# Performance work log

Hardware: AMD Instinct MI355X
Metric: run time of the kernel (lower is better)

## Reference

```python
import jax, jax.numpy as jnp
import numpy as np

EMB = 128
SQRT_EMB = 128 ** 0.5
LOGIT_CLIP = 10.0


def setup_inputs() -> dict:
    key = jax.random.key(0)
    ks = jax.random.split(key, 10)
    B, N, M, D = 128, 512, 512, EMB
    s = 1.0 / np.sqrt(D)
    return {
        "encoded_last_node": jax.random.normal(ks[0], (B, N, D), jnp.float32),
        "load": jax.random.uniform(ks[1], (B, N), jnp.float32),
        "cur_dist": jax.random.uniform(ks[2], (B, N, M), jnp.float32),
        "log_scale": jnp.ones((), jnp.float32),
        "ninf_mask": jnp.zeros((B, N, M), jnp.float32),
        "encoded_nodes": jax.random.normal(ks[3], (B, M, D), jnp.float32),
        "Wq_last": jax.random.normal(ks[4], (D, D + 1), jnp.float32) * s,
        "Wk": jax.random.normal(ks[5], (D, D), jnp.float32) * s,
        "Wv": jax.random.normal(ks[6], (D, D), jnp.float32) * s,
        "alpha1": jnp.ones((1,), jnp.float32),
        "alpha2": jnp.ones((1,), jnp.float32),
    }


def reference(encoded_last_node, load, cur_dist, log_scale, ninf_mask,
              encoded_nodes, Wq_last, Wk, Wv, alpha1, alpha2):
    # set_kv
    k = jnp.einsum('bmd,ed->bme', encoded_nodes, Wk)   # (B,M,D)
    v = jnp.einsum('bmd,ed->bme', encoded_nodes, Wv)   # (B,M,D)
    # query from last node + load
    input_cat = jnp.concatenate([encoded_last_node, load[:, :, None]], axis=2)  # (B,N,D+1)
    q = jnp.einsum('bnc,ec->bne', input_cat, Wq_last)  # (B,N,D)
    # AAFM: exp-bias linear attention with sigmoid gate
    adaptation_bias = -alpha1[0] * log_scale * cur_dist + ninf_mask  # (B,N,M)
    eb = jnp.exp(adaptation_bias)
    ek = jnp.exp(k)
    num = jnp.einsum('bnm,bmd->bnd', eb, ek * v)
    den = jnp.einsum('bnm,bmd->bnd', eb, ek)
    weighted = jnp.nan_to_num(num / den)  # mirrors torch nan_to_num correction
    aafm_out = jax.nn.sigmoid(q) * weighted  # (B,N,D)
    # single-head decode score against encoder embeddings
    score = jnp.einsum('bnd,bmd->bnm', aafm_out, encoded_nodes)
    score_scaled = score / SQRT_EMB - alpha2[0] * log_scale * cur_dist
    score_masked = LOGIT_CLIP * jnp.tanh(score_scaled) + ninf_mask
    probs = jax.nn.softmax(score_masked, axis=-1)
    return probs
```

## Files before the change

kernel.cpp:

```cpp
#include <hip/hip_runtime.h>
#include <math.h>

#define B 128
#define N 512
#define M 512
#define D 128

typedef __attribute__((ext_vector_type(8))) short s16x8;
typedef __attribute__((ext_vector_type(4))) short s16x4;
typedef __attribute__((ext_vector_type(4))) float f32x4;

#define MFMA16(a, b, c) __builtin_amdgcn_mfma_f32_16x16x32_bf16(a, b, c, 0, 0, 0)

__device__ __forceinline__ void gload16(const void* g, void* l) {
    __builtin_amdgcn_global_load_lds(
        (const __attribute__((address_space(1))) unsigned int*)g,
        (__attribute__((address_space(3))) unsigned int*)l, 16, 0, 0);
}

__device__ __forceinline__ float fast_tanh(float x) {
    x = fminf(fmaxf(x, -15.f), 15.f);
    float E = __expf(2.f * x);
    return 1.f - 2.f / (E + 1.f);
}

__device__ __forceinline__ unsigned short bf16rne(float x) {
    unsigned u = __float_as_uint(x);
    return (unsigned short)((u + 0x7FFF + ((u >> 16) & 1)) >> 16);
}

__device__ __forceinline__ void fsplit(float x, short& h, short& l) {
    unsigned u = __float_as_uint(x);
    h = (short)(u >> 16);
    float fh = __uint_as_float(u & 0xffff0000u);
    l = (short)(__float_as_uint(x - fh) >> 16);
}

__device__ __forceinline__ void fsplit8(float4 x0, float4 x1, s16x8& h, s16x8& l) {
    short a, b;
    fsplit(x0.x, a, b); h[0] = a; l[0] = b;
    fsplit(x0.y, a, b); h[1] = a; l[1] = b;
    fsplit(x0.z, a, b); h[2] = a; l[2] = b;
    fsplit(x0.w, a, b); h[3] = a; l[3] = b;
    fsplit(x1.x, a, b); h[4] = a; l[4] = b;
    fsplit(x1.y, a, b); h[5] = a; l[5] = b;
    fsplit(x1.z, a, b); h[6] = a; l[6] = b;
    fsplit(x1.w, a, b); h[7] = a; l[7] = b;
}

__device__ __forceinline__ void ebpack(float4 c0, float4 c1, float4 f0, float4 f1,
                                       float a1ls, s16x8& a) {
    a[0] = (short)bf16rne(__expf(fmaf(-a1ls, c0.x, f0.x)));
    a[1] = (short)bf16rne(__expf(fmaf(-a1ls, c0.y, f0.y)));
    a[2] = (short)bf16rne(__expf(fmaf(-a1ls, c0.z, f0.z)));
    a[3] = (short)bf16rne(__expf(fmaf(-a1ls, c0.w, f0.w)));
    a[4] = (short)bf16rne(__expf(fmaf(-a1ls, c1.x, f1.x)));
    a[5] = (short)bf16rne(__expf(fmaf(-a1ls, c1.y, f1.y)));
    a[6] = (short)bf16rne(__expf(fmaf(-a1ls, c1.z, f1.z)));
    a[7] = (short)bf16rne(__expf(fmaf(-a1ls, c1.w, f1.w)));
}

__global__ void k_prep_w(const float* __restrict__ Wk, const float* __restrict__ Wv,
                         const float* __restrict__ Wq,
                         unsigned short* __restrict__ Wk_hi, unsigned short* __restrict__ Wk_lo,
                         unsigned short* __restrict__ Wv_hi, unsigned short* __restrict__ Wv_lo,
                         unsigned short* __restrict__ Wq_hi, unsigned short* __restrict__ Wq_lo) {
    int i = blockIdx.x * 256 + threadIdx.x;
    short h, l;
    if (i < 16384) {
        fsplit(Wk[i], h, l); Wk_hi[i] = (unsigned short)h; Wk_lo[i] = (unsigned short)l;
    } else if (i < 32768) {
        int j = i - 16384;
        fsplit(Wv[j], h, l); Wv_hi[j] = (unsigned short)h; Wv_lo[j] = (unsigned short)l;
    } else {
        int j = i - 32768; int e = j >> 7, d = j & 127;
        fsplit(Wq[e * 129 + d], h, l); Wq_hi[j] = (unsigned short)h; Wq_lo[j] = (unsigned short)l;
    }
}

__global__ __launch_bounds__(256) void k_kv(const float* __restrict__ enc,
        const unsigned short* __restrict__ Wk_hi, const unsigned short* __restrict__ Wk_lo,
        const unsigned short* __restrict__ Wv_hi, const unsigned short* __restrict__ Wv_lo,
        unsigned short* __restrict__ EKb, unsigned short* __restrict__ EKVb) {
    int b = blockIdx.y;
    int wave = threadIdx.x >> 6, lane = threadIdx.x & 63;
    int row = lane & 15, kg = lane >> 4;
    int m0 = blockIdx.x * 64 + wave * 16;
    f32x4 acc[16];
#pragma unroll
    for (int i = 0; i < 16; i++) acc[i] = (f32x4)0.f;
    const float* ap = enc + ((size_t)b * M + m0 + row) * D + kg * 8;
#pragma unroll
    for (int ks = 0; ks < 4; ks++) {
        float4 x0 = *(const float4*)(ap + ks * 32);
        float4 x1 = *(const float4*)(ap + ks * 32 + 4);
        s16x8 ah, al;
        fsplit8(x0, x1, ah, al);
        int wb = ks * 32 + kg * 8;
#pragma unroll
        for (int ct = 0; ct < 8; ct++) {
            int e = ct * 16 + row;
            s16x8 bh = *(const s16x8*)(Wk_hi + e * D + wb);
            s16x8 bl = *(const s16x8*)(Wk_lo + e * D + wb);
            acc[ct] = MFMA16(ah, bh, acc[ct]);
            acc[ct] = MFMA16(al, bh, acc[ct]);
            acc[ct] = MFMA16(ah, bl, acc[ct]);
            bh = *(const s16x8*)(Wv_hi + e * D + wb);
            bl = *(const s16x8*)(Wv_lo + e * D + wb);
            acc[8 + ct] = MFMA16(ah, bh, acc[8 + ct]);
            acc[8 + ct] = MFMA16(al, bh, acc[8 + ct]);
            acc[8 + ct] = MFMA16(ah, bl, acc[8 + ct]);
        }
    }
#pragma unroll
    for (int ct = 0; ct < 8; ct++) {
        int e = ct * 16 + row;
        s16x4 kb, vb;
#pragma unroll
        for (int r = 0; r < 4; r++) {
            float ek = __expf(acc[ct][r]);
            float ev = ek * acc[8 + ct][r];
            kb[r] = (short)bf16rne(ek);
            vb[r] = (short)bf16rne(ev);
        }
        int m = m0 + kg * 4;
        int chunk = (m & 31) >> 3;
        int p = chunk ^ (e & 3);
        size_t o = ((size_t)b * D + e) * M + (size_t)(m & ~31) + p * 8 + (m & 7);
        *(s16x4*)(EKb + o) = kb;
        *(s16x4*)(EKVb + o) = vb;
    }
}

__global__ void k_encsplit(const float* __restrict__ enc,
                           unsigned short* __restrict__ Eh, unsigned short* __restrict__ El) {
    size_t i = (size_t)blockIdx.x * 256 + threadIdx.x;
    size_t bm = i >> 4;
    int c = (int)(i & 15);
    int m = (int)(bm & 511);
    int p = c ^ (m & 7);
    const float* src = enc + bm * 128 + c * 8;
    float4 x0 = *(const float4*)(src);
    float4 x1 = *(const float4*)(src + 4);
    s16x8 h, l;
    fsplit8(x0, x1, h, l);
    *(s16x8*)(Eh + bm * 128 + p * 8) = h;
    *(s16x8*)(El + bm * 128 + p * 8) = l;
}

__global__ __launch_bounds__(256, 3) void k_fused(
        const float* __restrict__ encl, const float* __restrict__ loadv,
        const float* __restrict__ Wq,
        const unsigned short* __restrict__ Wq_hi, const unsigned short* __restrict__ Wq_lo,
        const float* __restrict__ cd, const float* __restrict__ ninf,
        const unsigned short* __restrict__ EKVb, const unsigned short* __restrict__ EKb,
        const unsigned short* __restrict__ Eh, const unsigned short* __restrict__ El,
        const float* __restrict__ a1p, const float* __restrict__ a2p,
        const float* __restrict__ lsp, float* __restrict__ out) {
    int o = blockIdx.x;
    int xcd = o & 7, j = o >> 3;
    int b = ((j >> 4) << 3) + xcd;
    int nb = j & 15;
    int n0 = nb * 32;
    int w = threadIdx.x >> 6, lane = threadIdx.x & 63;
    int row = lane & 15, kg = lane >> 4;
    int ng = w >> 1, mh = w & 1;
    __shared__ __align__(16) char lds[2][16384];
    __shared__ float redm[32][2], reds[32][2];
    float a1ls = a1p[0] * lsp[0];
    float a2ls = a2p[0] * lsp[0];
    const float invs = 0.08838834764831845f;

    f32x4 sqa[2][2];
#pragma unroll
    for (int s = 0; s < 2; s++)
#pragma unroll
        for (int ct = 0; ct < 2; ct++) sqa[s][ct] = (f32x4)0.f;
#pragma unroll
    for (int s = 0; s < 2; s++) {
        const float* ap = encl + ((size_t)b * N + n0 + s * 16 + row) * D + kg * 8;
#pragma unroll
        for (int ks = 0; ks < 4; ks++) {
            float4 x0 = *(const float4*)(ap + ks * 32);
            float4 x1 = *(const float4*)(ap + ks * 32 + 4);
            s16x8 ah, al;
            fsplit8(x0, x1, ah, al);
            int wb = ks * 32 + kg * 8;
#pragma unroll
            for (int ct = 0; ct < 2; ct++) {
                int e = w * 32 + ct * 16 + row;
                s16x8 bh = *(const s16x8*)(Wq_hi + e * D + wb);
                s16x8 bl = *(const s16x8*)(Wq_lo + e * D + wb);
                sqa[s][ct] = MFMA16(ah, bh, sqa[s][ct]);
                sqa[s][ct] = MFMA16(al, bh, sqa[s][ct]);
                sqa[s][ct] = MFMA16(ah, bl, sqa[s][ct]);
            }
        }
    }
    float sqv[2][2][4];
#pragma unroll
    for (int s = 0; s < 2; s++)
#pragma unroll
        for (int ct = 0; ct < 2; ct++) {
            int e = w * 32 + ct * 16 + row;
            float wcol = Wq[e * 129 + 128];
#pragma unroll
            for (int r = 0; r < 4; r++) {
                int n = n0 + s * 16 + kg * 4 + r;
                float q = sqa[s][ct][r] + loadv[(size_t)b * N + n] * wcol;
                sqv[s][ct][r] = 1.f / (1.f + __expf(-q));
            }
        }

    f32x4 accN[2][2], accD[2][2];
#pragma unroll
    for (int s = 0; s < 2; s++)
#pragma unroll
        for (int i = 0; i < 2; i++) { accN[s][i] = (f32x4)0.f; accD[s][i] = (f32x4)0.f; }
    const char* gEKV = (const char*)EKVb + (size_t)b * D * M * 2;
    const char* gEK  = (const char*)EKb  + (size_t)b * D * M * 2;
    const float* cdp0 = cd + ((size_t)b * N + n0 + row) * M + kg * 8;
    const float* nfp0 = ninf + ((size_t)b * N + n0 + row) * M + kg * 8;
    const float* cdp1 = cdp0 + (size_t)16 * M;
    const float* nfp1 = nfp0 + (size_t)16 * M;
    int rbase = w * 2048 + row * 64 + ((kg ^ (row & 3)) << 4);

#define STAGE_ND(ldsbase, mt)                                                    \
    _Pragma("unroll")                                                            \
    for (int jv = 0; jv < 4; jv++) {                                             \
        int idx = jv * 256 + threadIdx.x;                                        \
        const char* gb = (idx >> 9) ? gEK : gEKV;                                \
        int rem = idx & 511;                                                     \
        gload16(gb + (size_t)(rem >> 2) * 1024 + (size_t)(mt) * 64 + (rem & 3) * 16, \
                (char*)(ldsbase) + idx * 16);                                    \
    }

    float4 c00 = *(const float4*)(cdp0), c01 = *(const float4*)(cdp0 + 4);
    float4 f00 = *(const float4*)(nfp0), f01 = *(const float4*)(nfp0 + 4);
    float4 c10 = *(const float4*)(cdp1), c11 = *(const float4*)(cdp1 + 4);
    float4 f10 = *(const float4*)(nfp1), f11 = *(const float4*)(nfp1 + 4);
    STAGE_ND((char*)lds, 0)

#pragma unroll 2
    for (int mt = 0; mt < 16; mt++) {
        int cur = mt & 1;
        __syncthreads();
        s16x8 a0, a1;
        ebpack(c00, c01, f00, f01, a1ls, a0);
        ebpack(c10, c11, f10, f11, a1ls, a1);
        if (mt < 15) {
            int m = (mt + 1) * 32;
            c00 = *(const float4*)(cdp0 + m); c01 = *(const float4*)(cdp0 + m + 4);
            f00 = *(const float4*)(nfp0 + m); f01 = *(const float4*)(nfp0 + m + 4);
            c10 = *(const float4*)(cdp1 + m); c11 = *(const float4*)(cdp1 + m + 4);
            f10 = *(const float4*)(nfp1 + m); f11 = *(const float4*)(nfp1 + m + 4);
            STAGE_ND((char*)lds + (cur ^ 1) * 16384, mt + 1)
        }
        const char* L = (const char*)lds + cur * 16384;
#pragma unroll
        for (int ct = 0; ct < 2; ct++) {
            int ro = ct * 1024 + rbase;
            s16x8 bv = *(const s16x8*)(L + ro);
            s16x8 bk = *(const s16x8*)(L + 8192 + ro);
            accN[0][ct] = MFMA16(a0, bv, accN[0][ct]);
            accN[1][ct] = MFMA16(a1, bv, accN[1][ct]);
            accD[0][ct] = MFMA16(a0, bk, accD[0][ct]);
            accD[1][ct] = MFMA16(a1, bk, accD[1][ct]);
        }
    }

    float* af = (float*)lds;
#pragma unroll
    for (int s = 0; s < 2; s++)
#pragma unroll
        for (int ct = 0; ct < 2; ct++) {
            int e = w * 32 + ct * 16 + row;
#pragma unroll
            for (int r = 0; r < 4; r++) {
                int nl = s * 16 + kg * 4 + r;
                float num = accN[s][ct][r], den = accD[s][ct][r];
                float ww = (den != 0.f) ? num / den : 0.f;
                float aafm = sqv[s][ct][r] * ww;
                unsigned u = __float_as_uint(aafm);
                unsigned hi = u >> 16;
                float fh = __uint_as_float(u & 0xffff0000u);
                unsigned lo = __float_as_uint(aafm - fh) >> 16;
                af[nl * 128 + e] = __uint_as_float(hi | (lo << 16));
            }
        }
    __syncthreads();
    s16x8 ah[4], al[4];
#pragma unroll
    for (int es = 0; es < 4; es++) {
        const float* src = af + (ng * 16 + row) * 128 + es * 32 + kg * 8;
        float4 w0 = *(const float4*)(src);
        float4 w1 = *(const float4*)(src + 4);
        unsigned u;
        u = __float_as_uint(w0.x); ah[es][0] = (short)(u & 0xffff); al[es][0] = (short)(u >> 16);
        u = __float_as_uint(w0.y); ah[es][1] = (short)(u & 0xffff); al[es][1] = (short)(u >> 16);
        u = __float_as_uint(w0.z); ah[es][2] = (short)(u & 0xffff); al[es][2] = (short)(u >> 16);
        u = __float_as_uint(w0.w); ah[es][3] = (short)(u & 0xffff); al[es][3] = (short)(u >> 16);
        u = __float_as_uint(w1.x); ah[es][4] = (short)(u & 0xffff); al[es][4] = (short)(u >> 16);
        u = __float_as_uint(w1.y); ah[es][5] = (short)(u & 0xffff); al[es][5] = (short)(u >> 16);
        u = __float_as_uint(w1.z); ah[es][6] = (short)(u & 0xffff); al[es][6] = (short)(u >> 16);
        u = __float_as_uint(w1.w); ah[es][7] = (short)(u & 0xffff); al[es][7] = (short)(u >> 16);
    }
    __syncthreads();

    f32x4 acc[16];
#pragma unroll
    for (int i = 0; i < 16; i++) acc[i] = (f32x4)0.f;
    int mloc = mh * 16 + row;
    int rb2 = mloc * 256;
    int sw = mloc & 7;
    size_t rowidx[4];
#pragma unroll
    for (int r = 0; r < 4; r++)
        rowidx[r] = ((size_t)b * N + n0 + ng * 16 + kg * 4 + r) * M;

#define STAGE_SC(ldsbase, mc)                                                      \
    _Pragma("unroll")                                                              \
    for (int jv = 0; jv < 4; jv++) {                                               \
        int id = (w * 4 + jv) * 64 + lane;                                         \
        int arr = id >> 9, rem = id & 511;                                         \
        const unsigned short* gb = arr ? El : Eh;                                  \
        gload16((const char*)gb + ((size_t)b * M + (size_t)(mc) * 32) * 256 + rem * 16, \
                (char*)(ldsbase) + arr * 8192 + rem * 16);                         \
    }

    STAGE_SC((char*)lds, 0)
#pragma unroll
    for (int mc = 0; mc < 16; mc++) {
        int cur = mc & 1;
        __syncthreads();
        const char* L = (const char*)lds + cur * 16384;
#pragma unroll
        for (int es = 0; es < 4; es++) {
            int ph = (4 * es + kg) ^ sw;
            s16x8 bh = *(const s16x8*)(L + rb2 + ph * 16);
            s16x8 bl = *(const s16x8*)(L + 8192 + rb2 + ph * 16);
            acc[mc] = MFMA16(ah[es], bh, acc[mc]);
            acc[mc] = MFMA16(al[es], bh, acc[mc]);
            acc[mc] = MFMA16(ah[es], bl, acc[mc]);
        }
        float cdv[4], nfv[4];
#pragma unroll
        for (int r = 0; r < 4; r++) {
            size_t idx = rowidx[r] + (size_t)mc * 32 + mloc;
            cdv[r] = cd[idx];
            nfv[r] = ninf[idx];
        }
        if (mc < 15) STAGE_SC((char*)lds + (cur ^ 1) * 16384, mc + 1)
#pragma unroll
        for (int r = 0; r < 4; r++) {
            acc[mc][r] = 10.f * fast_tanh(fmaf(acc[mc][r], invs, -a2ls * cdv[r]))
                       + nfv[r];
        }
    }
    float mx[4], sm[4];
#pragma unroll
    for (int r = 0; r < 4; r++) {
        float m = acc[0][r];
#pragma unroll
        for (int a = 1; a < 16; a++) m = fmaxf(m, acc[a][r]);
#pragma unroll
        for (int s = 1; s < 16; s <<= 1) m = fmaxf(m, __shfl_xor(m, s, 64));
        mx[r] = m;
    }
    int rl = ng * 16 + kg * 4;
    if (row == 0) {
#pragma unroll
        for (int r = 0; r < 4; r++) redm[rl + r][mh] = mx[r];
    }
    __syncthreads();
#pragma unroll
    for (int r = 0; r < 4; r++) {
        float m = fmaxf(redm[rl + r][0], redm[rl + r][1]);
        float s = 0.f;
#pragma unroll
        for (int a = 0; a < 16; a++) {
            float e = __expf(acc[a][r] - m);
            acc[a][r] = e;
            s += e;
        }
#pragma unroll
        for (int sh = 1; sh < 16; sh <<= 1) s += __shfl_xor(s, sh, 64);
        sm[r] = s;
    }
    if (row == 0) {
#pragma unroll
        for (int r = 0; r < 4; r++) reds[rl + r][mh] = sm[r];
    }
    __syncthreads();
#pragma unroll
    for (int r = 0; r < 4; r++) {
        float inv = 1.f / (reds[rl + r][0] + reds[rl + r][1]);
        size_t ro = ((size_t)b * N + n0 + rl + r) * M;
#pragma unroll
        for (int a = 0; a < 16; a++) {
            out[ro + a * 32 + mh * 16 + row] = acc[a][r] * inv;
        }
    }
}

extern "C" void kernel_launch(void* const* d_in, const int* in_sizes, int n_in,
                              void* d_out, int out_size, void* d_ws, size_t ws_size,
                              hipStream_t stream) {
    const float* encl  = (const float*)d_in[0];
    const float* loadv = (const float*)d_in[1];
    const float* cdist = (const float*)d_in[2];
    const float* ls    = (const float*)d_in[3];
    const float* ninf  = (const float*)d_in[4];
    const float* enc   = (const float*)d_in[5];
    const float* Wq    = (const float*)d_in[6];
    const float* Wk    = (const float*)d_in[7];
    const float* Wv    = (const float*)d_in[8];
    const float* a1    = (const float*)d_in[9];
    const float* a2    = (const float*)d_in[10];
    char* ws = (char*)d_ws;
    unsigned short* EKb     = (unsigned short*)(ws);
    unsigned short* EKVb    = (unsigned short*)(ws + 16777216);
    unsigned short* ENC_hi  = (unsigned short*)(ws + 33554432);
    unsigned short* ENC_lo  = (unsigned short*)(ws + 50331648);
    unsigned short* Wk_hi   = (unsigned short*)(ws + 67108864);
    unsigned short* Wk_lo   = (unsigned short*)(ws + 67108864 + 32768);
    unsigned short* Wv_hi   = (unsigned short*)(ws + 67108864 + 65536);
    unsigned short* Wv_lo   = (unsigned short*)(ws + 67108864 + 98304);
    unsigned short* Wq_hi   = (unsigned short*)(ws + 67108864 + 131072);
    unsigned short* Wq_lo   = (unsigned short*)(ws + 67108864 + 163840);
    float* out = (float*)d_out;

    k_prep_w<<<192, 256, 0, stream>>>(Wk, Wv, Wq, Wk_hi, Wk_lo, Wv_hi, Wv_lo, Wq_hi, Wq_lo);
    k_kv<<<dim3(8, 128), 256, 0, stream>>>(enc, Wk_hi, Wk_lo, Wv_hi, Wv_lo, EKb, EKVb);
    k_encsplit<<<4096, 256, 0, stream>>>(enc, ENC_hi, ENC_lo);
    k_fused<<<2048, 256, 0, stream>>>(encl, loadv, Wq, Wq_hi, Wq_lo,
                                      cdist, ninf, EKVb, EKb, ENC_hi, ENC_lo,
                                      a1, a2, ls, out);
}
```

Before: 363.1 us.

## Use per-wave LDS staging with manual vmcnt pipelining and single-bf16 encoder operand

Each wave now owns a private LDS slice and stages its own tiles with a two-deep prefetch, synchronised by explicit s_waitcnt vmcnt/lgkmcnt counts instead of block-wide __syncthreads in both the attention and score loops. The score phase is repartitioned so each wave handles all 32 rows over its own 128-column slice. The encoder embedding is packed to a single bf16 copy rather than a hi/lo split, which drops one MFMA per step and halves the staged bytes. This lowers the precision of the score matmul, and the hand-counted waitcnt values are fragile if the compiler reorders memory operations.

```diff
diff --git a/kernel.cpp b/kernel.cpp
--- a/kernel.cpp
+++ b/kernel.cpp
@@ -11,6 +11,14 @@
 typedef __attribute__((ext_vector_type(4))) float f32x4;
 
 #define MFMA16(a, b, c) __builtin_amdgcn_mfma_f32_16x16x32_bf16(a, b, c, 0, 0, 0)
+
+#define FENCE()   asm volatile("" ::: "memory")
+#define VMCNT4()  asm volatile("s_waitcnt vmcnt(4)" ::: "memory")
+#define VMCNT8()  asm volatile("s_waitcnt vmcnt(8)" ::: "memory")
+#define VMCNT12() asm volatile("s_waitcnt vmcnt(12)" ::: "memory")
+#define VMCNT20() asm volatile("s_waitcnt vmcnt(20)" ::: "memory")
+#define LGKMCNT0() asm volatile("s_waitcnt lgkmcnt(0)" ::: "memory")
+#define SCHEDBAR() __builtin_amdgcn_sched_barrier(0)
 
 __device__ __forceinline__ void gload16(const void* g, void* l) {
     __builtin_amdgcn_global_load_lds(
@@ -132,8 +140,7 @@
     }
 }
 
-__global__ void k_encsplit(const float* __restrict__ enc,
-                           unsigned short* __restrict__ Eh, unsigned short* __restrict__ El) {
+__global__ void k_encpack(const float* __restrict__ enc, unsigned short* __restrict__ Eb) {
     size_t i = (size_t)blockIdx.x * 256 + threadIdx.x;
     size_t bm = i >> 4;
     int c = (int)(i & 15);
@@ -142,10 +149,12 @@
     const float* src = enc + bm * 128 + c * 8;
     float4 x0 = *(const float4*)(src);
     float4 x1 = *(const float4*)(src + 4);
-    s16x8 h, l;
-    fsplit8(x0, x1, h, l);
-    *(s16x8*)(Eh + bm * 128 + p * 8) = h;
-    *(s16x8*)(El + bm * 128 + p * 8) = l;
+    s16x8 v;
+    v[0] = (short)bf16rne(x0.x); v[1] = (short)bf16rne(x0.y);
+    v[2] = (short)bf16rne(x0.z); v[3] = (short)bf16rne(x0.w);
+    v[4] = (short)bf16rne(x1.x); v[5] = (short)bf16rne(x1.y);
+    v[6] = (short)bf16rne(x1.z); v[7] = (short)bf16rne(x1.w);
+    *(s16x8*)(Eb + bm * 128 + p * 8) = v;
 }
 
 __global__ __launch_bounds__(256, 3) void k_fused(
@@ -154,7 +163,7 @@
         const unsigned short* __restrict__ Wq_hi, const unsigned short* __restrict__ Wq_lo,
         const float* __restrict__ cd, const float* __restrict__ ninf,
         const unsigned short* __restrict__ EKVb, const unsigned short* __restrict__ EKb,
-        const unsigned short* __restrict__ Eh, const unsigned short* __restrict__ El,
+        const unsigned short* __restrict__ Eb,
         const float* __restrict__ a1p, const float* __restrict__ a2p,
         const float* __restrict__ lsp, float* __restrict__ out) {
     int o = blockIdx.x;
@@ -164,12 +173,12 @@
     int n0 = nb * 32;
     int w = threadIdx.x >> 6, lane = threadIdx.x & 63;
     int row = lane & 15, kg = lane >> 4;
-    int ng = w >> 1, mh = w & 1;
-    __shared__ __align__(16) char lds[2][16384];
-    __shared__ float redm[32][2], reds[32][2];
+    __shared__ __align__(16) char lds[32768];
+    __shared__ float redm[32][4], reds[32][4];
     float a1ls = a1p[0] * lsp[0];
     float a2ls = a2p[0] * lsp[0];
     const float invs = 0.08838834764831845f;
+    char* wb = lds + w * 8192;
 
     f32x4 sqa[2][2];
 #pragma unroll
@@ -185,12 +194,12 @@
             float4 x1 = *(const float4*)(ap + ks * 32 + 4);
             s16x8 ah, al;
             fsplit8(x0, x1, ah, al);
-            int wb = ks * 32 + kg * 8;
+            int wqo = ks * 32 + kg * 8;
 #pragma unroll
             for (int ct = 0; ct < 2; ct++) {
                 int e = w * 32 + ct * 16 + row;
-                s16x8 bh = *(const s16x8*)(Wq_hi + e * D + wb);
-                s16x8 bl = *(const s16x8*)(Wq_lo + e * D + wb);
+                s16x8 bh = *(const s16x8*)(Wq_hi + e * D + wqo);
+                s16x8 bl = *(const s16x8*)(Wq_lo + e * D + wqo);
                 sqa[s][ct] = MFMA16(ah, bh, sqa[s][ct]);
                 sqa[s][ct] = MFMA16(al, bh, sqa[s][ct]);
                 sqa[s][ct] = MFMA16(ah, bl, sqa[s][ct]);
@@ -211,6 +220,7 @@
                 sqv[s][ct][r] = 1.f / (1.f + __expf(-q));
             }
         }
+    FENCE();
 
     f32x4 accN[2][2], accD[2][2];
 #pragma unroll
@@ -223,52 +233,63 @@
     const float* nfp0 = ninf + ((size_t)b * N + n0 + row) * M + kg * 8;
     const float* cdp1 = cdp0 + (size_t)16 * M;
     const float* nfp1 = nfp0 + (size_t)16 * M;
-    int rbase = w * 2048 + row * 64 + ((kg ^ (row & 3)) << 4);
-
-#define STAGE_ND(ldsbase, mt)                                                    \
+
+#define STAGE_B(bufptr, mt)                                                      \
     _Pragma("unroll")                                                            \
     for (int jv = 0; jv < 4; jv++) {                                             \
-        int idx = jv * 256 + threadIdx.x;                                        \
-        const char* gb = (idx >> 9) ? gEK : gEKV;                                \
-        int rem = idx & 511;                                                     \
-        gload16(gb + (size_t)(rem >> 2) * 1024 + (size_t)(mt) * 64 + (rem & 3) * 16, \
-                (char*)(ldsbase) + idx * 16);                                    \
-    }
-
-    float4 c00 = *(const float4*)(cdp0), c01 = *(const float4*)(cdp0 + 4);
-    float4 f00 = *(const float4*)(nfp0), f01 = *(const float4*)(nfp0 + 4);
-    float4 c10 = *(const float4*)(cdp1), c11 = *(const float4*)(cdp1 + 4);
-    float4 f10 = *(const float4*)(nfp1), f11 = *(const float4*)(nfp1 + 4);
-    STAGE_ND((char*)lds, 0)
-
-#pragma unroll 2
+        int arr = jv >> 1;                                                       \
+        int rem = (jv & 1) * 64 + lane;                                          \
+        const char* gb = arr ? gEK : gEKV;                                       \
+        gload16(gb + (size_t)(w * 32 + (rem >> 2)) * 1024 + (size_t)(mt) * 64 +  \
+                    (rem & 3) * 16,                                              \
+                (char*)(bufptr) + arr * 2048 + rem * 16);                        \
+    }
+
+    float4 Ac[2][2][2], Af[2][2][2];
+#define LOAD_A(p, mt)                                                            \
+    Ac[p][0][0] = *(const float4*)(cdp0 + (mt) * 32);                            \
+    Ac[p][0][1] = *(const float4*)(cdp0 + (mt) * 32 + 4);                        \
+    Af[p][0][0] = *(const float4*)(nfp0 + (mt) * 32);                            \
+    Af[p][0][1] = *(const float4*)(nfp0 + (mt) * 32 + 4);                        \
+    Ac[p][1][0] = *(const float4*)(cdp1 + (mt) * 32);                            \
+    Ac[p][1][1] = *(const float4*)(cdp1 + (mt) * 32 + 4);                        \
+    Af[p][1][0] = *(const float4*)(nfp1 + (mt) * 32);                            \
+    Af[p][1][1] = *(const float4*)(nfp1 + (mt) * 32 + 4);
+
+    LOAD_A(0, 0) FENCE();
+    STAGE_B(wb, 0) FENCE();
+    LOAD_A(1, 1) FENCE();
+    STAGE_B(wb + 4096, 1) FENCE();
+
+    int rbB = row * 64 + ((kg ^ (row & 3)) << 4);
+#pragma unroll
     for (int mt = 0; mt < 16; mt++) {
-        int cur = mt & 1;
-        __syncthreads();
+        if (mt < 2) { VMCNT12(); } else if (mt < 15) { VMCNT20(); } else { VMCNT8(); }
+        SCHEDBAR();
+        int p = mt & 1;
         s16x8 a0, a1;
-        ebpack(c00, c01, f00, f01, a1ls, a0);
-        ebpack(c10, c11, f10, f11, a1ls, a1);
-        if (mt < 15) {
-            int m = (mt + 1) * 32;
-            c00 = *(const float4*)(cdp0 + m); c01 = *(const float4*)(cdp0 + m + 4);
-            f00 = *(const float4*)(nfp0 + m); f01 = *(const float4*)(nfp0 + m + 4);
-            c10 = *(const float4*)(cdp1 + m); c11 = *(const float4*)(cdp1 + m + 4);
-            f10 = *(const float4*)(nfp1 + m); f11 = *(const float4*)(nfp1 + m + 4);
-            STAGE_ND((char*)lds + (cur ^ 1) * 16384, mt + 1)
-        }
-        const char* L = (const char*)lds + cur * 16384;
+        ebpack(Ac[p][0][0], Ac[p][0][1], Af[p][0][0], Af[p][0][1], a1ls, a0);
+        ebpack(Ac[p][1][0], Ac[p][1][1], Af[p][1][0], Af[p][1][1], a1ls, a1);
+        const char* L = wb + p * 4096;
 #pragma unroll
         for (int ct = 0; ct < 2; ct++) {
-            int ro = ct * 1024 + rbase;
+            int ro = ct * 1024 + rbB;
             s16x8 bv = *(const s16x8*)(L + ro);
-            s16x8 bk = *(const s16x8*)(L + 8192 + ro);
+            s16x8 bk = *(const s16x8*)(L + 2048 + ro);
             accN[0][ct] = MFMA16(a0, bv, accN[0][ct]);
             accN[1][ct] = MFMA16(a1, bv, accN[1][ct]);
             accD[0][ct] = MFMA16(a0, bk, accD[0][ct]);
             accD[1][ct] = MFMA16(a1, bk, accD[1][ct]);
         }
-    }
-
+        if (mt <= 13) {
+            LGKMCNT0();
+            SCHEDBAR();
+            STAGE_B(wb + p * 4096, mt + 2) FENCE();
+            LOAD_A(p, mt + 2) FENCE();
+        }
+    }
+
+    __syncthreads();
     float* af = (float*)lds;
 #pragma unroll
     for (int s = 0; s < 2; s++)
@@ -289,118 +310,141 @@
             }
         }
     __syncthreads();
-    s16x8 ah[4], al[4];
-#pragma unroll
-    for (int es = 0; es < 4; es++) {
-        const float* src = af + (ng * 16 + row) * 128 + es * 32 + kg * 8;
-        float4 w0 = *(const float4*)(src);
-        float4 w1 = *(const float4*)(src + 4);
-        unsigned u;
-        u = __float_as_uint(w0.x); ah[es][0] = (short)(u & 0xffff); al[es][0] = (short)(u >> 16);
-        u = __float_as_uint(w0.y); ah[es][1] = (short)(u & 0xffff); al[es][1] = (short)(u >> 16);
-        u = __float_as_uint(w0.z); ah[es][2] = (short)(u & 0xffff); al[es][2] = (short)(u >> 16);
-        u = __float_as_uint(w0.w); ah[es][3] = (short)(u & 0xffff); al[es][3] = (short)(u >> 16);
-        u = __float_as_uint(w1.x); ah[es][4] = (short)(u & 0xffff); al[es][4] = (short)(u >> 16);
-        u = __float_as_uint(w1.y); ah[es][5] = (short)(u & 0xffff); al[es][5] = (short)(u >> 16);
-        u = __float_as_uint(w1.z); ah[es][6] = (short)(u & 0xffff); al[es][6] = (short)(u >> 16);
-        u = __float_as_uint(w1.w); ah[es][7] = (short)(u & 0xffff); al[es][7] = (short)(u >> 16);
-    }
+    s16x8 ah[2][4], al[2][4];
+#pragma unroll
+    for (int s = 0; s < 2; s++)
+#pragma unroll
+        for (int es = 0; es < 4; es++) {
+            const float* src = af + (s * 16 + row) * 128 + es * 32 + kg * 8;
+            float4 w0 = *(const float4*)(src);
+            float4 w1 = *(const float4*)(src + 4);
+            unsigned u;
+            u = __float_as_uint(w0.x); ah[s][es][0] = (short)(u & 0xffff); al[s][es][0] = (short)(u >> 16);
+            u = __float_as_uint(w0.y); ah[s][es][1] = (short)(u & 0xffff); al[s][es][1] = (short)(u >> 16);
+            u = __float_as_uint(w0.z); ah[s][es][2] = (short)(u & 0xffff); al[s][es][2] = (short)(u >> 16);
+            u = __float_as_uint(w0.w); ah[s][es][3] = (short)(u & 0xffff); al[s][es][3] = (short)(u >> 16);
+            u = __float_as_uint(w1.x); ah[s][es][4] = (short)(u & 0xffff); al[s][es][4] = (short)(u >> 16);
+            u = __float_as_uint(w1.y); ah[s][es][5] = (short)(u & 0xffff); al[s][es][5] = (short)(u >> 16);
+            u = __float_as_uint(w1.z); ah[s][es][6] = (short)(u & 0xffff); al[s][es][6] = (short)(u >> 16);
+            u = __float_as_uint(w1.w); ah[s][es][7] = (short)(u & 0xffff); al[s][es][7] = (short)(u >> 16);
+        }
     __syncthreads();
-
-    f32x4 acc[16];
-#pragma unroll
-    for (int i = 0; i < 16; i++) acc[i] = (f32x4)0.f;
-    int mloc = mh * 16 + row;
-    int rb2 = mloc * 256;
-    int sw = mloc & 7;
-    size_t rowidx[4];
-#pragma unroll
-    for (int r = 0; r < 4; r++)
-        rowidx[r] = ((size_t)b * N + n0 + ng * 16 + kg * 4 + r) * M;
-
-#define STAGE_SC(ldsbase, mc)                                                      \
-    _Pragma("unroll")                                                              \
-    for (int jv = 0; jv < 4; jv++) {                                               \
-        int id = (w * 4 + jv) * 64 + lane;                                         \
-        int arr = id >> 9, rem = id & 511;                                         \
-        const unsigned short* gb = arr ? El : Eh;                                  \
-        gload16((const char*)gb + ((size_t)b * M + (size_t)(mc) * 32) * 256 + rem * 16, \
-                (char*)(ldsbase) + arr * 8192 + rem * 16);                         \
-    }
-
-    STAGE_SC((char*)lds, 0)
-#pragma unroll
-    for (int mc = 0; mc < 16; mc++) {
-        int cur = mc & 1;
-        __syncthreads();
-        const char* L = (const char*)lds + cur * 16384;
+    FENCE();
+
+    f32x4 acc[2][8];
+#pragma unroll
+    for (int s = 0; s < 2; s++)
+#pragma unroll
+        for (int p = 0; p < 8; p++) acc[s][p] = (f32x4)0.f;
+    const char* gEb = (const char*)Eb + (size_t)b * M * 256;
+
+#define STAGE_D(bufptr, p)                                                       \
+    _Pragma("unroll")                                                            \
+    for (int jv = 0; jv < 4; jv++) {                                             \
+        int id = jv * 64 + lane;                                                 \
+        gload16(gEb + (size_t)(w * 128 + (p) * 16 + (id >> 4)) * 256 + (id & 15) * 16, \
+                (char*)(bufptr) + id * 16);                                      \
+    }
+
+    STAGE_D(wb, 0) FENCE();
+    STAGE_D(wb + 4096, 1) FENCE();
+
+#pragma unroll
+    for (int p = 0; p < 8; p++) {
+        if (p == 0) { VMCNT4(); } else if (p < 7) { VMCNT12(); } else { VMCNT8(); }
+        SCHEDBAR();
+        float cdv[2][4], nfv[2][4];
+#pragma unroll
+        for (int s = 0; s < 2; s++)
+#pragma unroll
+            for (int r = 0; r < 4; r++) {
+                size_t idx = ((size_t)b * N + n0 + s * 16 + kg * 4 + r) * M
+                           + (size_t)w * 128 + (size_t)p * 16 + row;
+                cdv[s][r] = cd[idx];
+                nfv[s][r] = ninf[idx];
+            }
+        FENCE();
+        const char* L = wb + (p & 1) * 4096;
+        int sw = row & 7;
 #pragma unroll
         for (int es = 0; es < 4; es++) {
             int ph = (4 * es + kg) ^ sw;
-            s16x8 bh = *(const s16x8*)(L + rb2 + ph * 16);
-            s16x8 bl = *(const s16x8*)(L + 8192 + rb2 + ph * 16);
-            acc[mc] = MFMA16(ah[es], bh, acc[mc]);
-            acc[mc] = MFMA16(al[es], bh, acc[mc]);
-            acc[mc] = MFMA16(ah[es], bl, acc[mc]);
-        }
-        float cdv[4], nfv[4];
+            s16x8 bb = *(const s16x8*)(L + row * 256 + ph * 16);
+            acc[0][p] = MFMA16(ah[0][es], bb, acc[0][p]);
+            acc[0][p] = MFMA16(al[0][es], bb, acc[0][p]);
+            acc[1][p] = MFMA16(ah[1][es], bb, acc[1][p]);
+            acc[1][p] = MFMA16(al[1][es], bb, acc[1][p]);
+        }
+        if (p <= 5) {
+            LGKMCNT0();
+            SCHEDBAR();
+            STAGE_D(wb + (p & 1) * 4096, p + 2) FENCE();
+        }
+#pragma unroll
+        for (int s = 0; s < 2; s++)
+#pragma unroll
+            for (int r = 0; r < 4; r++) {
+                acc[s][p][r] = 10.f * fast_tanh(fmaf(acc[s][p][r], invs, -a2ls * cdv[s][r]))
+                             + nfv[s][r];
+            }
+    }
+
+    float mx[2][4], sm[2][4];
+#pragma unroll
+    for (int s = 0; s < 2; s++)
 #pragma unroll
         for (int r = 0; r < 4; r++) {
-            size_t idx = rowidx[r] + (size_t)mc * 32 + mloc;
-            cdv[r] = cd[idx];
-            nfv[r] = ninf[idx];
-        }
-        if (mc < 15) STAGE_SC((char*)lds + (cur ^ 1) * 16384, mc + 1)
+            float m = acc[s][0][r];
+#pragma unroll
+            for (int p = 1; p < 8; p++) m = fmaxf(m, acc[s][p][r]);
+#pragma unroll
+            for (int sh = 1; sh < 16; sh <<= 1) m = fmaxf(m, __shfl_xor(m, sh, 64));
+            mx[s][r] = m;
+        }
+    if (row == 0) {
+#pragma unroll
+        for (int s = 0; s < 2; s++)
+#pragma unroll
+            for (int r = 0; r < 4; r++) redm[s * 16 + kg * 4 + r][w] = mx[s][r];
+    }
+    __syncthreads();
+#pragma unroll
+    for (int s = 0; s < 2; s++)
 #pragma unroll
         for (int r = 0; r < 4; r++) {
-            acc[mc][r] = 10.f * fast_tanh(fmaf(acc[mc][r], invs, -a2ls * cdv[r]))
-                       + nfv[r];
-        }
-    }
-    float mx[4], sm[4];
-#pragma unroll
-    for (int r = 0; r < 4; r++) {
-        float m = acc[0][r];
-#pragma unroll
-        for (int a = 1; a < 16; a++) m = fmaxf(m, acc[a][r]);
-#pragma unroll
-        for (int s = 1; s < 16; s <<= 1) m = fmaxf(m, __shfl_xor(m, s, 64));
-        mx[r] = m;
-    }
-    int rl = ng * 16 + kg * 4;
+            int nl = s * 16 + kg * 4 + r;
+            float m = fmaxf(fmaxf(redm[nl][0], redm[nl][1]),
+                            fmaxf(redm[nl][2], redm[nl][3]));
+            float sum = 0.f;
+#pragma unroll
+            for (int p = 0; p < 8; p++) {
+                float e = __expf(acc[s][p][r] - m);
+                acc[s][p][r] = e;
+                sum += e;
+            }
+#pragma unroll
+            for (int sh = 1; sh < 16; sh <<= 1) sum += __shfl_xor(sum, sh, 64);
+            sm[s][r] = sum;
+        }
     if (row == 0) {
 #pragma unroll
-        for (int r = 0; r < 4; r++) redm[rl + r][mh] = mx[r];
+        for (int s = 0; s < 2; s++)
+#pragma unroll
+            for (int r = 0; r < 4; r++) reds[s * 16 + kg * 4 + r][w] = sm[s][r];
     }
     __syncthreads();
 #pragma unroll
-    for (int r = 0; r < 4; r++) {
-        float m = fmaxf(redm[rl + r][0], redm[rl + r][1]);
-        float s = 0.f;
-#pragma unroll
-        for (int a = 0; a < 16; a++) {
-            float e = __expf(acc[a][r] - m);
-            acc[a][r] = e;
-            s += e;
-        }
-#pragma unroll
-        for (int sh = 1; sh < 16; sh <<= 1) s += __shfl_xor(s, sh, 64);
-        sm[r] = s;
-    }
-    if (row == 0) {
-#pragma unroll
-        for (int r = 0; r < 4; r++) reds[rl + r][mh] = sm[r];
-    }
-    __syncthreads();
-#pragma unroll
-    for (int r = 0; r < 4; r++) {
-        float inv = 1.f / (reds[rl + r][0] + reds[rl + r][1]);
-        size_t ro = ((size_t)b * N + n0 + rl + r) * M;
-#pragma unroll
-        for (int a = 0; a < 16; a++) {
-            out[ro + a * 32 + mh * 16 + row] = acc[a][r] * inv;
-        }
-    }
+    for (int s = 0; s < 2; s++)
+#pragma unroll
+        for (int r = 0; r < 4; r++) {
+            int nl = s * 16 + kg * 4 + r;
+            float inv = 1.f / (reds[nl][0] + reds[nl][1] + reds[nl][2] + reds[nl][3]);
+            size_t ro = ((size_t)b * N + n0 + nl) * M + (size_t)w * 128 + row;
+#pragma unroll
+            for (int p = 0; p < 8; p++) {
+                out[ro + p * 16] = acc[s][p][r] * inv;
+            }
+        }
 }
 
 extern "C" void kernel_launch(void* const* d_in, const int* in_sizes, int n_in,
@@ -420,20 +464,19 @@
     char* ws = (char*)d_ws;
     unsigned short* EKb     = (unsigned short*)(ws);
     unsigned short* EKVb    = (unsigned short*)(ws + 16777216);
-    unsigned short* ENC_hi  = (unsigned short*)(ws + 33554432);
-    unsigned short* ENC_lo  = (unsigned short*)(ws + 50331648);
-    unsigned short* Wk_hi   = (unsigned short*)(ws + 67108864);
-    unsigned short* Wk_lo   = (unsigned short*)(ws + 67108864 + 32768);
-    unsigned short* Wv_hi   = (unsigned short*)(ws + 67108864 + 65536);
-    unsigned short* Wv_lo   = (unsigned short*)(ws + 67108864 + 98304);
-    unsigned short* Wq_hi   = (unsigned short*)(ws + 67108864 + 131072);
-    unsigned short* Wq_lo   = (unsigned short*)(ws + 67108864 + 163840);
+    unsigned short* Eb      = (unsigned short*)(ws + 33554432);
+    unsigned short* Wk_hi   = (unsigned short*)(ws + 50331648);
+    unsigned short* Wk_lo   = (unsigned short*)(ws + 50331648 + 32768);
+    unsigned short* Wv_hi   = (unsigned short*)(ws + 50331648 + 65536);
+    unsigned short* Wv_lo   = (unsigned short*)(ws + 50331648 + 98304);
+    unsigned short* Wq_hi   = (unsigned short*)(ws + 50331648 + 131072);
+    unsigned short* Wq_lo   = (unsigned short*)(ws + 50331648 + 163840);
     float* out = (float*)d_out;
 
     k_prep_w<<<192, 256, 0, stream>>>(Wk, Wv, Wq, Wk_hi, Wk_lo, Wv_hi, Wv_lo, Wq_hi, Wq_lo);
     k_kv<<<dim3(8, 128), 256, 0, stream>>>(enc, Wk_hi, Wk_lo, Wv_hi, Wv_lo, EKb, EKVb);
-    k_encsplit<<<4096, 256, 0, stream>>>(enc, ENC_hi, ENC_lo);
+    k_encpack<<<4096, 256, 0, stream>>>(enc, Eb);
     k_fused<<<2048, 256, 0, stream>>>(encl, loadv, Wq, Wq_hi, Wq_lo,
-                                      cdist, ninf, EKVb, EKb, ENC_hi, ENC_lo,
+                                      cdist, ninf, EKVb, EKb, Eb,
                                       a1, a2, ls, out);
 }
```

New measurement: 350.9 us. -3.4%, faster.
